# Performance work log

Hardware: AMD Instinct MI355X
Metric: run time of the kernel (lower is better)

The kernel has to match this reference:

```python
import jax, jax.numpy as jnp
import numpy as np

N, T, S, D = 50000, 8192, 16, 64
DIN = 4 * D + 3  # MLP input dim
LEAKY = 0.001


def setup_inputs() -> dict:
    key = jax.random.key(0)
    ks = jax.random.split(key, 12)
    coords = jax.random.normal(ks[0], (N, S, 3), dtype=jnp.float32)
    encoded = jax.random.normal(ks[1], (N, D), dtype=jnp.float32)
    t = jax.random.uniform(ks[2], (S,), dtype=jnp.float32)
    answer = jax.random.normal(ks[3], (N, S, 3), dtype=jnp.float32)
    # tetras: 4 distinct atom indices + chirality sign (+/-1)
    base = jax.random.randint(ks[4], (T,), 0, N - 4)
    idx4 = base[:, None] + jnp.arange(4, dtype=jnp.int32)[None, :]
    sign = 2 * jax.random.randint(ks[5], (T, 1), 0, 2) - 1
    tetras = jnp.concatenate([idx4.astype(jnp.int32), sign.astype(jnp.int32)], axis=1)
    # MLP params (Linear(DIN,D), Linear(D,D), Linear(D,D), Linear(D,2))
    def lin(k, fi, fo):
        b = 1.0 / np.sqrt(fi)
        return jax.random.uniform(k, (fi, fo), jnp.float32, -b, b)
    W1 = lin(ks[6], DIN, D); b1 = jnp.zeros((D,), jnp.float32)
    W2 = lin(ks[7], D, D);   b2 = jnp.zeros((D,), jnp.float32)
    W3 = lin(ks[8], D, D);   b3 = jnp.zeros((D,), jnp.float32)
    W4 = lin(ks[9], D, 2);   b4 = jnp.zeros((2,), jnp.float32)
    return {"coords": coords, "tetras": tetras, "encoded": encoded, "t": t,
            "answer": answer, "W1": W1, "b1": b1, "W2": W2, "b2": b2,
            "W3": W3, "b3": b3, "W4": W4, "b4": b4}


def _lrelu(x):
    return jnp.where(x >= 0, x, LEAKY * x)


def reference(coords, tetras, encoded, t, answer, W1, b1, W2, b2, W3, b3, W4, b4):
    # permutations: [3T, 5]
    perms = jnp.concatenate([tetras,
                             tetras[:, jnp.array([0, 3, 1, 2, 4])],
                             tetras[:, jnp.array([0, 2, 3, 1, 4])]], axis=0)
    idx = perms[:, :4]                      # [3T, 4]
    p = coords[idx]                         # [3T, 4, S, 3]
    v0 = p[:, 1] - p[:, 0]                  # [3T, S, 3]
    v1 = p[:, 2] - p[:, 0]
    v2 = p[:, 3] - p[:, 0]
    sign = perms[:, 4].astype(coords.dtype)[:, None, None]
    cross = sign * jnp.cross(v1, v2)        # [3T, S, 3]
    cross = cross / jnp.linalg.norm(cross, axis=-1, keepdims=True)
    sm = v1 + v2
    sm = sm / jnp.linalg.norm(sm, axis=-1, keepdims=True)
    out = jnp.sum(cross * v0, axis=-1)      # [3T, S]
    along = -jnp.sum(sm * v0, axis=-1)      # [3T, S]

    enc = encoded[idx]                      # [3T, 4, D]
    P = perms.shape[0]
    Sn = t.shape[0]
    feats = jnp.concatenate([
        jnp.broadcast_to(enc[:, 0][:, None, :], (P, Sn, D)),
        jnp.broadcast_to(enc[:, 1][:, None, :], (P, Sn, D)),
        jnp.broadcast_to(enc[:, 2][:, None, :], (P, Sn, D)),
        jnp.broadcast_to(enc[:, 3][:, None, :], (P, Sn, D)),
        jnp.broadcast_to(t[None, :, None], (P, Sn, 1)),
        out[:, :, None] / 4,
        along[:, :, None] / 4,
    ], axis=2)                              # [3T, S, 4D+3]

    h = _lrelu(feats @ W1 + b1)
    h = _lrelu(h @ W2 + b2)
    h = _lrelu(h @ W3 + b3)
    delta = h @ W4 + b4                     # [3T, S, 2]

    answer = answer.at[perms[:, 0]].add(-0.25 * delta[:, :, 0:1] * cross)
    answer = answer.at[perms[:, 1]].add(0.25 * delta[:, :, 1:2] * cross)
    return answer
```

## Files before the change

kernel.cpp:

```cpp
#include <hip/hip_runtime.h>

#define TT 8192
#define SS 16
#define DD 64
#define LEAKY 0.001f
#define PERMS (3*TT)
#define WPB 4
#define PPW 12
#define NBLK (PERMS/(WPB*PPW))

typedef short  short8 __attribute__((ext_vector_type(8)));
typedef __bf16 bf16x8 __attribute__((ext_vector_type(8)));
typedef float  f32x4  __attribute__((ext_vector_type(4)));

union FragU { short8 s; bf16x8 b; };

__device__ __forceinline__ void wave_sync() {
  asm volatile("s_waitcnt lgkmcnt(0)" ::: "memory");
}
__device__ __forceinline__ short f2bf_rne(float x) {
  unsigned u = __builtin_bit_cast(unsigned, x);
  return (short)((u + 0x7FFFu + ((u >> 16) & 1u)) >> 16);
}
__device__ __forceinline__ short f2bf_fast(float x) {
  unsigned u = __builtin_bit_cast(unsigned, x);
  return (short)((u + 0x8000u) >> 16);
}
__device__ __forceinline__ float bf2f(short v) {
  return __builtin_bit_cast(float, ((unsigned)(unsigned short)v) << 16);
}
__device__ __forceinline__ float lrelu(float x) { return x >= 0.f ? x : LEAKY * x; }

__global__ __launch_bounds__(WPB*64)
void tetra_mlp_kernel(const float* __restrict__ coords,
                      const int*   __restrict__ tetras,
                      const float* __restrict__ encoded,
                      const float* __restrict__ tvec,
                      const float* __restrict__ W1, const float* __restrict__ b1,
                      const float* __restrict__ W2, const float* __restrict__ b2,
                      const float* __restrict__ W3, const float* __restrict__ b3,
                      const float* __restrict__ W4, const float* __restrict__ b4,
                      float* __restrict__ answer)
{
  __shared__ __align__(16) short w2f[8][64][8];
  __shared__ __align__(16) short w3f[8][64][8];
  __shared__ __align__(16) float w4cols[DD][2];
  __shared__ __align__(16) float w1r[3][DD];
  __shared__ int   idxs_[WPB][PPW*5];
  __shared__ __align__(16) short bases_[WPB][PPW*DD];
  __shared__ __align__(16) short hs_[WPB][1024];
  __shared__ short crs_[WPB][4*SS*3];
  __shared__ __align__(4) unsigned short oas_[WPB][4*SS*2];
  __shared__ float dls_[WPB][SS*2];

  const int tid = threadIdx.x;

  for (int e = tid; e < 8*64; e += WPB*64) {
    const int f = e >> 6, ln = e & 63;
    const int kg2 = ln >> 4, n2 = ln & 15;
    const int ks = f >> 2, nt = f & 3;
    const int base = (ks*32 + kg2*8)*DD + nt*16 + n2;
    #pragma unroll
    for (int j = 0; j < 8; ++j) {
      w2f[f][ln][j] = f2bf_rne(W2[base + j*DD]);
      w3f[f][ln][j] = f2bf_rne(W3[base + j*DD]);
    }
  }
  if (tid < DD*2) w4cols[tid >> 1][tid & 1] = W4[tid];
  if (tid < 3*DD) w1r[tid >> 6][tid & 63] = W1[256*DD + tid];
  __syncthreads();

  const int wv = tid >> 6, lane = tid & 63;
  const int kg = lane >> 4, n16 = lane & 15;
  int*   idxw = idxs_[wv];
  short* basw = bases_[wv];
  short* hsw  = hs_[wv];
  short* crw  = crs_[wv];
  unsigned short* oaw = oas_[wv];
  float* dlw  = dls_[wv];

  const float ts_l = tvec[n16];
  float b1v[4], b2v[4], b3v[4];
  #pragma unroll
  for (int nt = 0; nt < 4; ++nt) {
    b1v[nt] = b1[nt*16 + n16];
    b2v[nt] = b2[nt*16 + n16];
    b3v[nt] = b3[nt*16 + n16];
  }
  const float b40 = b4[0], b41 = b4[1];

  const int permBase = (blockIdx.x*WPB + wv)*PPW;

  if (lane < PPW) {
    const int perm = permBase + lane;
    const int tet = perm & (TT-1), v = perm >> 13;
    const int* tp = tetras + tet*5;
    const int i0 = tp[0], i1 = tp[1], i2 = tp[2], i3 = tp[3], sg = tp[4];
    int b, c, d;
    if (v == 0)      { b = i1; c = i2; d = i3; }
    else if (v == 1) { b = i3; c = i1; d = i2; }
    else             { b = i2; c = i3; d = i1; }
    int* ip = &idxw[lane*5];
    ip[0] = i0; ip[1] = b; ip[2] = c; ip[3] = d; ip[4] = sg;
  }
  wave_sync();

  {
    f32x4 bD[4];
    #pragma unroll
    for (int nt = 0; nt < 4; ++nt) bD[nt] = (f32x4){b1v[nt], b1v[nt], b1v[nt], b1v[nt]};
    #pragma unroll
    for (int r = 0; r < 4; ++r) {
      #pragma unroll
      for (int ks = 0; ks < 2; ++ks) {
        FragU af;
        if (n16 < PPW) {
          const float* ep = encoded + (size_t)idxw[n16*5 + r]*DD + ks*32 + kg*8;
          const float4 e0 = *(const float4*)ep;
          const float4 e1 = *(const float4*)(ep + 4);
          af.s = (short8){f2bf_fast(e0.x), f2bf_fast(e0.y), f2bf_fast(e0.z), f2bf_fast(e0.w),
                          f2bf_fast(e1.x), f2bf_fast(e1.y), f2bf_fast(e1.z), f2bf_fast(e1.w)};
        } else {
          af.s = (short8){0,0,0,0,0,0,0,0};
        }
        const float* wp = W1 + (size_t)(r*64 + ks*32 + kg*8)*DD + n16;
        #pragma unroll
        for (int nt = 0; nt < 4; ++nt) {
          const float* wq = wp + nt*16;
          FragU bfr;
          #pragma unroll
          for (int j = 0; j < 8; ++j) bfr.s[j] = f2bf_rne(wq[j*DD]);
          bD[nt] = __builtin_amdgcn_mfma_f32_16x16x32_bf16(af.b, bfr.b, bD[nt], 0, 0, 0);
        }
      }
    }
    #pragma unroll
    for (int nt = 0; nt < 4; ++nt)
      #pragma unroll
      for (int r = 0; r < 4; ++r) {
        const int prow = kg*4 + r;
        if (prow < PPW) basw[prow*DD + nt*16 + n16] = f2bf_fast(bD[nt][r]);
      }
  }
  wave_sync();

  #pragma unroll 1
  for (int pi = 0; pi < PPW; ++pi) {
    if ((pi & 3) == 0) {
      wave_sync();
      const int pp = pi + kg;
      const int* ip = &idxw[pp*5];
      const int ga = ip[0], gb = ip[1], gc = ip[2], gd = ip[3];
      const float sg = (float)ip[4];
      const int s2 = n16;
      const float* pa = coords + ((size_t)ga*SS + s2)*3;
      const float* pb = coords + ((size_t)gb*SS + s2)*3;
      const float* pc = coords + ((size_t)gc*SS + s2)*3;
      const float* pd = coords + ((size_t)gd*SS + s2)*3;
      const float ax = pa[0], ay = pa[1], az = pa[2];
      const float v0x = pb[0]-ax, v0y = pb[1]-ay, v0z = pb[2]-az;
      const float v1x = pc[0]-ax, v1y = pc[1]-ay, v1z = pc[2]-az;
      const float v2x = pd[0]-ax, v2y = pd[1]-ay, v2z = pd[2]-az;
      float cx = (v1y*v2z - v1z*v2y)*sg;
      float cy = (v1z*v2x - v1x*v2z)*sg;
      float cz = (v1x*v2y - v1y*v2x)*sg;
      const float rc = rsqrtf(cx*cx + cy*cy + cz*cz);
      cx *= rc; cy *= rc; cz *= rc;
      float sx = v1x+v2x, sy = v1y+v2y, sz = v1z+v2z;
      const float rs = rsqrtf(sx*sx + sy*sy + sz*sz);
      sx *= rs; sy *= rs; sz *= rs;
      const float outv =   cx*v0x + cy*v0y + cz*v0z;
      const float alng = -(sx*v0x + sy*v0y + sz*v0z);
      const int oo = kg*SS + s2;
      crw[oo*3+0] = f2bf_rne(cx);
      crw[oo*3+1] = f2bf_rne(cy);
      crw[oo*3+2] = f2bf_rne(cz);
      oaw[oo*2+0] = (unsigned short)f2bf_rne(outv*0.25f);
      oaw[oo*2+1] = (unsigned short)f2bf_rne(alng*0.25f);
      wave_sync();
    }

    const int s = n16;

    FragU a1[2];
    {
      const int ob = ((pi & 3)*SS + s)*2;
      const float o0 = bf2f((short)oaw[ob+0]);
      const float o1 = bf2f((short)oaw[ob+1]);
      #pragma unroll
      for (int ks = 0; ks < 2; ++ks) {
        const short8 bb = *(const short8*)&basw[pi*DD + ks*32 + kg*8];
        FragU af;
        #pragma unroll
        for (int q = 0; q < 2; ++q) {
          const int ko = ks*32 + kg*8 + q*4;
          const float4 wt = *(const float4*)&w1r[0][ko];
          const float4 wo = *(const float4*)&w1r[1][ko];
          const float4 wa = *(const float4*)&w1r[2][ko];
          #pragma unroll
          for (int j = 0; j < 4; ++j) {
            const float x = bf2f(bb[q*4+j]) + ts_l*wt[j] + o0*wo[j] + o1*wa[j];
            af.s[q*4+j] = f2bf_fast(lrelu(x));
          }
        }
        a1[ks] = af;
      }
    }

    f32x4 d2[4];
    #pragma unroll
    for (int nt = 0; nt < 4; ++nt) d2[nt] = (f32x4){b2v[nt], b2v[nt], b2v[nt], b2v[nt]};
    #pragma unroll
    for (int ks = 0; ks < 2; ++ks)
      #pragma unroll
      for (int nt = 0; nt < 4; ++nt) {
        FragU wf; wf.s = *(const short8*)&w2f[ks*4+nt][lane][0];
        d2[nt] = __builtin_amdgcn_mfma_f32_16x16x32_bf16(a1[ks].b, wf.b, d2[nt], 0, 0, 0);
      }
    #pragma unroll
    for (int nt = 0; nt < 4; ++nt)
      #pragma unroll
      for (int r = 0; r < 4; ++r) {
        const int row = kg*4 + r;
        const int colB = nt*32 + n16*2;
        hsw[(row*128 + (colB ^ ((row & 7) << 4))) >> 1] = f2bf_fast(lrelu(d2[nt][r]));
      }
    wave_sync();

    FragU a2[2];
    #pragma unroll
    for (int ks = 0; ks < 2; ++ks) {
      const int off = s*128 + ((ks*64 + kg*16) ^ ((s & 7) << 4));
      a2[ks].s = *(const short8*)((const char*)hsw + off);
    }
    f32x4 d3[4];
    #pragma unroll
    for (int nt = 0; nt < 4; ++nt) d3[nt] = (f32x4){b3v[nt], b3v[nt], b3v[nt], b3v[nt]};
    #pragma unroll
    for (int ks = 0; ks < 2; ++ks)
      #pragma unroll
      for (int nt = 0; nt < 4; ++nt) {
        FragU wf; wf.s = *(const short8*)&w3f[ks*4+nt][lane][0];
        d3[nt] = __builtin_amdgcn_mfma_f32_16x16x32_bf16(a2[ks].b, wf.b, d3[nt], 0, 0, 0);
      }
    #pragma unroll
    for (int nt = 0; nt < 4; ++nt)
      #pragma unroll
      for (int r = 0; r < 4; ++r) {
        const int row = kg*4 + r;
        const int colB = nt*32 + n16*2;
        hsw[(row*128 + (colB ^ ((row & 7) << 4))) >> 1] = f2bf_fast(lrelu(d3[nt][r]));
      }
    wave_sync();

    float dd0 = 0.f, dd1 = 0.f;
    #pragma unroll
    for (int half = 0; half < 2; ++half) {
      const int off = s*128 + ((kg*32 + half*16) ^ ((s & 7) << 4));
      const short8 hv = *(const short8*)((const char*)hsw + off);
      #pragma unroll
      for (int j = 0; j < 8; ++j) {
        const int k = kg*16 + half*8 + j;
        const float h = bf2f(hv[j]);
        dd0 = fmaf(h, w4cols[k][0], dd0);
        dd1 = fmaf(h, w4cols[k][1], dd1);
      }
    }
    dd0 += __shfl_xor(dd0, 16, 64); dd0 += __shfl_xor(dd0, 32, 64);
    dd1 += __shfl_xor(dd1, 16, 64); dd1 += __shfl_xor(dd1, 32, 64);
    if (lane < SS) { dlw[lane*2+0] = dd0 + b40; dlw[lane*2+1] = dd1 + b41; }
    wave_sync();

    const int ta = idxw[pi*5+0], tb = idxw[pi*5+1];
    #pragma unroll
    for (int rr = 0; rr < 2; ++rr) {
      const int e = lane + rr*64;
      if (e < SS*6) {
        const int ss2 = e/6, k2 = e - ss2*6;
        const int hi = (k2 >= 3) ? 1 : 0, comp = k2 - hi*3;
        const float val = (hi ? 0.25f : -0.25f) * dlw[ss2*2+hi]
                        * bf2f(crw[((pi & 3)*SS + ss2)*3 + comp]);
        const int tgt = hi ? tb : ta;
        unsafeAtomicAdd(answer + ((size_t)tgt*SS + ss2)*3 + comp, val);
      }
    }
  }
}

extern "C" void kernel_launch(void* const* d_in, const int* in_sizes, int n_in,
                              void* d_out, int out_size, void* d_ws, size_t ws_size,
                              hipStream_t stream) {
  const float* coords  = (const float*)d_in[0];
  const int*   tetras  = (const int*)d_in[1];
  const float* encoded = (const float*)d_in[2];
  const float* tvec    = (const float*)d_in[3];
  const float* answer  = (const float*)d_in[4];
  const float* W1 = (const float*)d_in[5];
  const float* b1 = (const float*)d_in[6];
  const float* W2 = (const float*)d_in[7];
  const float* b2 = (const float*)d_in[8];
  const float* W3 = (const float*)d_in[9];
  const float* b3 = (const float*)d_in[10];
  const float* W4 = (const float*)d_in[11];
  const float* b4 = (const float*)d_in[12];
  float* out = (float*)d_out;

  hipMemcpyAsync(out, answer, sizeof(float)*(size_t)out_size,
                 hipMemcpyDeviceToDevice, stream);
  tetra_mlp_kernel<<<NBLK, WPB*64, 0, stream>>>(coords, tetras, encoded, tvec,
                                                W1, b1, W2, b2, W3, b3, W4, b4, out);
}
```

Before: 48.44 us.

## Halve perms per wave, share layer-1 base across block, MFMA final layer

Each wave now handles 6 permutations instead of 12, which doubles the grid size and adds a min-blocks launch bound for occupancy. The layer-1 encoded-feature GEMM is computed by two waves for all 24 block permutations and shared through LDS behind a block barrier. All geometry for a wave is precomputed up front instead of every 4 iterations. The W1 tail rows and W4 are held in registers as bf16 fragments, and the final 64->2 projection runs as MFMA instead of a scalar dot product with shuffles. The trade-off is that two waves sit idle during the layer-1 GEMM, W2/W3 staging is repeated across twice as many blocks, and rounding W1-tail and W4 weights to bf16 adds some precision loss.

```diff
diff --git a/kernel.cpp b/kernel.cpp
--- a/kernel.cpp
+++ b/kernel.cpp
@@ -6,8 +6,9 @@
 #define LEAKY 0.001f
 #define PERMS (3*TT)
 #define WPB 4
-#define PPW 12
-#define NBLK (PERMS/(WPB*PPW))
+#define PPW 6
+#define BPB (WPB*PPW)
+#define NBLK (PERMS/BPB)
 
 typedef short  short8 __attribute__((ext_vector_type(8)));
 typedef __bf16 bf16x8 __attribute__((ext_vector_type(8)));
@@ -31,7 +32,7 @@
 }
 __device__ __forceinline__ float lrelu(float x) { return x >= 0.f ? x : LEAKY * x; }
 
-__global__ __launch_bounds__(WPB*64)
+__global__ __launch_bounds__(WPB*64, 4)
 void tetra_mlp_kernel(const float* __restrict__ coords,
                       const int*   __restrict__ tetras,
                       const float* __restrict__ encoded,
@@ -44,13 +45,11 @@
 {
   __shared__ __align__(16) short w2f[8][64][8];
   __shared__ __align__(16) short w3f[8][64][8];
-  __shared__ __align__(16) float w4cols[DD][2];
-  __shared__ __align__(16) float w1r[3][DD];
-  __shared__ int   idxs_[WPB][PPW*5];
-  __shared__ __align__(16) short bases_[WPB][PPW*DD];
+  __shared__ int   idxs[BPB*5];
+  __shared__ __align__(16) short bases[BPB*DD];
   __shared__ __align__(16) short hs_[WPB][1024];
-  __shared__ short crs_[WPB][4*SS*3];
-  __shared__ __align__(4) unsigned short oas_[WPB][4*SS*2];
+  __shared__ short crs_[WPB][PPW*SS*3];
+  __shared__ __align__(4) unsigned short oas_[WPB][PPW*SS*2];
   __shared__ float dls_[WPB][SS*2];
 
   const int tid = threadIdx.x;
@@ -66,90 +65,57 @@
       w3f[f][ln][j] = f2bf_rne(W3[base + j*DD]);
     }
   }
-  if (tid < DD*2) w4cols[tid >> 1][tid & 1] = W4[tid];
-  if (tid < 3*DD) w1r[tid >> 6][tid & 63] = W1[256*DD + tid];
-  __syncthreads();
-
-  const int wv = tid >> 6, lane = tid & 63;
-  const int kg = lane >> 4, n16 = lane & 15;
-  int*   idxw = idxs_[wv];
-  short* basw = bases_[wv];
-  short* hsw  = hs_[wv];
-  short* crw  = crs_[wv];
-  unsigned short* oaw = oas_[wv];
-  float* dlw  = dls_[wv];
-
-  const float ts_l = tvec[n16];
-  float b1v[4], b2v[4], b3v[4];
-  #pragma unroll
-  for (int nt = 0; nt < 4; ++nt) {
-    b1v[nt] = b1[nt*16 + n16];
-    b2v[nt] = b2[nt*16 + n16];
-    b3v[nt] = b3[nt*16 + n16];
-  }
-  const float b40 = b4[0], b41 = b4[1];
-
-  const int permBase = (blockIdx.x*WPB + wv)*PPW;
-
-  if (lane < PPW) {
-    const int perm = permBase + lane;
-    const int tet = perm & (TT-1), v = perm >> 13;
+  if (tid < BPB) {
+    const int gp = blockIdx.x*BPB + tid;
+    const int tet = gp & (TT-1), v = gp >> 13;
     const int* tp = tetras + tet*5;
     const int i0 = tp[0], i1 = tp[1], i2 = tp[2], i3 = tp[3], sg = tp[4];
     int b, c, d;
     if (v == 0)      { b = i1; c = i2; d = i3; }
     else if (v == 1) { b = i3; c = i1; d = i2; }
     else             { b = i2; c = i3; d = i1; }
-    int* ip = &idxw[lane*5];
+    int* ip = &idxs[tid*5];
     ip[0] = i0; ip[1] = b; ip[2] = c; ip[3] = d; ip[4] = sg;
   }
-  wave_sync();
-
-  {
-    f32x4 bD[4];
-    #pragma unroll
-    for (int nt = 0; nt < 4; ++nt) bD[nt] = (f32x4){b1v[nt], b1v[nt], b1v[nt], b1v[nt]};
-    #pragma unroll
-    for (int r = 0; r < 4; ++r) {
-      #pragma unroll
-      for (int ks = 0; ks < 2; ++ks) {
-        FragU af;
-        if (n16 < PPW) {
-          const float* ep = encoded + (size_t)idxw[n16*5 + r]*DD + ks*32 + kg*8;
-          const float4 e0 = *(const float4*)ep;
-          const float4 e1 = *(const float4*)(ep + 4);
-          af.s = (short8){f2bf_fast(e0.x), f2bf_fast(e0.y), f2bf_fast(e0.z), f2bf_fast(e0.w),
-                          f2bf_fast(e1.x), f2bf_fast(e1.y), f2bf_fast(e1.z), f2bf_fast(e1.w)};
-        } else {
-          af.s = (short8){0,0,0,0,0,0,0,0};
-        }
-        const float* wp = W1 + (size_t)(r*64 + ks*32 + kg*8)*DD + n16;
-        #pragma unroll
-        for (int nt = 0; nt < 4; ++nt) {
-          const float* wq = wp + nt*16;
-          FragU bfr;
-          #pragma unroll
-          for (int j = 0; j < 8; ++j) bfr.s[j] = f2bf_rne(wq[j*DD]);
-          bD[nt] = __builtin_amdgcn_mfma_f32_16x16x32_bf16(af.b, bfr.b, bD[nt], 0, 0, 0);
-        }
-      }
-    }
-    #pragma unroll
-    for (int nt = 0; nt < 4; ++nt)
-      #pragma unroll
-      for (int r = 0; r < 4; ++r) {
-        const int prow = kg*4 + r;
-        if (prow < PPW) basw[prow*DD + nt*16 + n16] = f2bf_fast(bD[nt][r]);
-      }
-  }
-  wave_sync();
-
-  #pragma unroll 1
-  for (int pi = 0; pi < PPW; ++pi) {
-    if ((pi & 3) == 0) {
-      wave_sync();
-      const int pp = pi + kg;
-      const int* ip = &idxw[pp*5];
+  __syncthreads();
+
+  const int wv = tid >> 6, lane = tid & 63;
+  const int kg = lane >> 4, n16 = lane & 15;
+  short* hsw = hs_[wv];
+  short* crw = crs_[wv];
+  unsigned short* oaw = oas_[wv];
+  float* dlw = dls_[wv];
+
+  const float ts_l = tvec[n16];
+  float b2v[4], b3v[4];
+  #pragma unroll
+  for (int nt = 0; nt < 4; ++nt) { b2v[nt] = b2[nt*16 + n16]; b3v[nt] = b3[nt*16 + n16]; }
+  const float b40 = b4[0], b41 = b4[1];
+
+  FragU w1t_[2], w1o_[2], w1a_[2];
+  #pragma unroll
+  for (int ks = 0; ks < 2; ++ks)
+    #pragma unroll
+    for (int j = 0; j < 8; ++j) {
+      const int k = ks*32 + kg*8 + j;
+      w1t_[ks].s[j] = f2bf_rne(W1[256*DD + k]);
+      w1o_[ks].s[j] = f2bf_rne(W1[257*DD + k]);
+      w1a_[ks].s[j] = f2bf_rne(W1[258*DD + k]);
+    }
+  FragU wf4[2];
+  #pragma unroll
+  for (int ks = 0; ks < 2; ++ks)
+    #pragma unroll
+    for (int j = 0; j < 8; ++j) {
+      const int k = ks*32 + kg*8 + j;
+      wf4[ks].s[j] = (n16 < 2) ? f2bf_rne(W4[k*2 + n16]) : (short)0;
+    }
+
+  #pragma unroll
+  for (int pass = 0; pass < 2; ++pass) {
+    const int lp = pass*4 + kg;
+    if (lp < PPW) {
+      const int* ip = &idxs[(wv*PPW + lp)*5];
       const int ga = ip[0], gb = ip[1], gc = ip[2], gd = ip[3];
       const float sg = (float)ip[4];
       const int s2 = n16;
@@ -171,37 +137,77 @@
       sx *= rs; sy *= rs; sz *= rs;
       const float outv =   cx*v0x + cy*v0y + cz*v0z;
       const float alng = -(sx*v0x + sy*v0y + sz*v0z);
-      const int oo = kg*SS + s2;
+      const int oo = lp*SS + s2;
       crw[oo*3+0] = f2bf_rne(cx);
       crw[oo*3+1] = f2bf_rne(cy);
       crw[oo*3+2] = f2bf_rne(cz);
       oaw[oo*2+0] = (unsigned short)f2bf_rne(outv*0.25f);
       oaw[oo*2+1] = (unsigned short)f2bf_rne(alng*0.25f);
-      wave_sync();
-    }
-
+    }
+  }
+  wave_sync();
+
+  if (wv < 2) {
+    f32x4 bD[4];
+    #pragma unroll
+    for (int nt = 0; nt < 4; ++nt) {
+      const float bv = b1[nt*16 + n16];
+      bD[nt] = (f32x4){bv, bv, bv, bv};
+    }
+    #pragma unroll
+    for (int r = 0; r < 4; ++r) {
+      #pragma unroll
+      for (int ks = 0; ks < 2; ++ks) {
+        FragU af;
+        if (n16 < 12) {
+          const float* ep = encoded + (size_t)idxs[(wv*12 + n16)*5 + r]*DD + ks*32 + kg*8;
+          const float4 e0 = *(const float4*)ep;
+          const float4 e1 = *(const float4*)(ep + 4);
+          af.s = (short8){f2bf_fast(e0.x), f2bf_fast(e0.y), f2bf_fast(e0.z), f2bf_fast(e0.w),
+                          f2bf_fast(e1.x), f2bf_fast(e1.y), f2bf_fast(e1.z), f2bf_fast(e1.w)};
+        } else {
+          af.s = (short8){0,0,0,0,0,0,0,0};
+        }
+        const float* wp = W1 + (size_t)(r*64 + ks*32 + kg*8)*DD + n16;
+        #pragma unroll
+        for (int nt = 0; nt < 4; ++nt) {
+          const float* wq = wp + nt*16;
+          FragU bfr;
+          #pragma unroll
+          for (int j = 0; j < 8; ++j) bfr.s[j] = f2bf_rne(wq[j*DD]);
+          bD[nt] = __builtin_amdgcn_mfma_f32_16x16x32_bf16(af.b, bfr.b, bD[nt], 0, 0, 0);
+        }
+      }
+    }
+    #pragma unroll
+    for (int nt = 0; nt < 4; ++nt)
+      #pragma unroll
+      for (int r = 0; r < 4; ++r) {
+        const int prow = kg*4 + r;
+        if (prow < 12) bases[(wv*12 + prow)*DD + nt*16 + n16] = f2bf_fast(bD[nt][r]);
+      }
+  }
+  __syncthreads();
+
+  #pragma unroll 1
+  for (int pi = 0; pi < PPW; ++pi) {
     const int s = n16;
+    const int bp = wv*PPW + pi;
 
     FragU a1[2];
     {
-      const int ob = ((pi & 3)*SS + s)*2;
+      const int ob = (pi*SS + s)*2;
       const float o0 = bf2f((short)oaw[ob+0]);
       const float o1 = bf2f((short)oaw[ob+1]);
       #pragma unroll
       for (int ks = 0; ks < 2; ++ks) {
-        const short8 bb = *(const short8*)&basw[pi*DD + ks*32 + kg*8];
+        const short8 bb = *(const short8*)&bases[bp*DD + ks*32 + kg*8];
         FragU af;
         #pragma unroll
-        for (int q = 0; q < 2; ++q) {
-          const int ko = ks*32 + kg*8 + q*4;
-          const float4 wt = *(const float4*)&w1r[0][ko];
-          const float4 wo = *(const float4*)&w1r[1][ko];
-          const float4 wa = *(const float4*)&w1r[2][ko];
-          #pragma unroll
-          for (int j = 0; j < 4; ++j) {
-            const float x = bf2f(bb[q*4+j]) + ts_l*wt[j] + o0*wo[j] + o1*wa[j];
-            af.s[q*4+j] = f2bf_fast(lrelu(x));
-          }
+        for (int j = 0; j < 8; ++j) {
+          const float x = bf2f(bb[j]) + ts_l*bf2f(w1t_[ks].s[j])
+                        + o0*bf2f(w1o_[ks].s[j]) + o1*bf2f(w1a_[ks].s[j]);
+          af.s[j] = f2bf_fast(lrelu(x));
         }
         a1[ks] = af;
       }
@@ -253,25 +259,27 @@
       }
     wave_sync();
 
-    float dd0 = 0.f, dd1 = 0.f;
-    #pragma unroll
-    for (int half = 0; half < 2; ++half) {
-      const int off = s*128 + ((kg*32 + half*16) ^ ((s & 7) << 4));
-      const short8 hv = *(const short8*)((const char*)hsw + off);
-      #pragma unroll
-      for (int j = 0; j < 8; ++j) {
-        const int k = kg*16 + half*8 + j;
-        const float h = bf2f(hv[j]);
-        dd0 = fmaf(h, w4cols[k][0], dd0);
-        dd1 = fmaf(h, w4cols[k][1], dd1);
-      }
-    }
-    dd0 += __shfl_xor(dd0, 16, 64); dd0 += __shfl_xor(dd0, 32, 64);
-    dd1 += __shfl_xor(dd1, 16, 64); dd1 += __shfl_xor(dd1, 32, 64);
-    if (lane < SS) { dlw[lane*2+0] = dd0 + b40; dlw[lane*2+1] = dd1 + b41; }
+    FragU a3[2];
+    #pragma unroll
+    for (int ks = 0; ks < 2; ++ks) {
+      const int off = s*128 + ((ks*64 + kg*16) ^ ((s & 7) << 4));
+      a3[ks].s = *(const short8*)((const char*)hsw + off);
+    }
+    f32x4 d4 = (f32x4){0.f, 0.f, 0.f, 0.f};
+    {
+      const float binit = (n16 == 0) ? b40 : ((n16 == 1) ? b41 : 0.f);
+      d4 = (f32x4){binit, binit, binit, binit};
+    }
+    #pragma unroll
+    for (int ks = 0; ks < 2; ++ks)
+      d4 = __builtin_amdgcn_mfma_f32_16x16x32_bf16(a3[ks].b, wf4[ks].b, d4, 0, 0, 0);
+    if (n16 < 2) {
+      #pragma unroll
+      for (int r = 0; r < 4; ++r) dlw[(kg*4 + r)*2 + n16] = d4[r];
+    }
     wave_sync();
 
-    const int ta = idxw[pi*5+0], tb = idxw[pi*5+1];
+    const int ta = idxs[bp*5+0], tb = idxs[bp*5+1];
     #pragma unroll
     for (int rr = 0; rr < 2; ++rr) {
       const int e = lane + rr*64;
@@ -279,11 +287,12 @@
         const int ss2 = e/6, k2 = e - ss2*6;
         const int hi = (k2 >= 3) ? 1 : 0, comp = k2 - hi*3;
         const float val = (hi ? 0.25f : -0.25f) * dlw[ss2*2+hi]
-                        * bf2f(crw[((pi & 3)*SS + ss2)*3 + comp]);
+                        * bf2f(crw[(pi*SS + ss2)*3 + comp]);
         const int tgt = hi ? tb : ta;
         unsafeAtomicAdd(answer + ((size_t)tgt*SS + ss2)*3 + comp, val);
       }
     }
+    wave_sync();
   }
 }
 
```

New measurement: 75.82 us. 56.5% more time.
